# Kernel tuning notes

Hardware: AMD Instinct MI355X
Metric: run time of the kernel (lower is better)

The kernel has to match this reference:

```python
import jax, jax.numpy as jnp
import numpy as np

DT = 0.01  # init kwarg dt
M = 501    # microstructure feature length (hardcoded split [501, 501] in source)
H = 128    # hidden width


def _mlp(x, W1, b1, W2, b2):
    # Linear -> Softplus -> Linear
    return jax.nn.softplus(x @ W1 + b1) @ W2 + b2


def _linear_init(key, fan_in, fan_out):
    k1, k2 = jax.random.split(key)
    s = 1.0 / np.sqrt(fan_in)
    W = jax.random.uniform(k1, (fan_in, fan_out), minval=-s, maxval=s, dtype=jnp.float32)
    b = jax.random.uniform(k2, (fan_out,), minval=-s, maxval=s, dtype=jnp.float32)
    return W, b


def setup_inputs() -> dict:
    key = jax.random.key(0)
    ks = jax.random.split(key, 10)
    B, T = 32768, 512
    Ew1, Eb1 = _linear_init(ks[0], 2 * M, H)   # energy net: Linear(1002,128)
    Ew2, Eb2 = _linear_init(ks[1], H, 1)
    nw1, nb1 = _linear_init(ks[2], M, H)       # nu net: Linear(501,128)
    nw2, nb2 = _linear_init(ks[3], H, 1)
    bw1, bb1 = _linear_init(ks[4], 2 * M, H)   # beta net: Linear(1002,128)
    bw2, bb2 = _linear_init(ks[5], H, 1)
    e = jax.random.normal(ks[6], (B, T, 1), dtype=jnp.float32) * 0.01
    e_dot = jax.random.normal(ks[7], (B, T, 1), dtype=jnp.float32) * 0.01
    E = jax.random.uniform(ks[8], (B, M), dtype=jnp.float32)
    nu = jax.random.uniform(ks[9], (B, M), dtype=jnp.float32)
    return dict(e=e, e_dot=e_dot, E=E, nu=nu,
                Ew1=Ew1, Eb1=Eb1, Ew2=Ew2, Eb2=Eb2,
                nw1=nw1, nb1=nb1, nw2=nw2, nb2=nb2,
                bw1=bw1, bb1=bb1, bw2=bw2, bb2=bb2)


def reference(e, e_dot, E, nu,
              Ew1, Eb1, Ew2, Eb2,
              nw1, nb1, nw2, nb2,
              bw1, bb1, bw2, bb2):
    # microstructure encoder: m = concat(E, nu) -> [B, 1002]; constant over time,
    # so the three small MLPs are evaluated ONCE (the per-step autograd.grad of the
    # quadratic energy/dissipation potentials has closed form).
    m = jnp.concatenate((E, nu), axis=-1)
    Emod = jnp.exp(_mlp(m, Ew1, Eb1, Ew2, Eb2))                              # exp(E(m))    [B,1]
    nu_feat = m[:, M:]                                                        # second half of split
    nuv = jnp.exp(jnp.square(_mlp(nu_feat, nw1, nb1, nw2, nb2)) / 40000.0)    # exp(nu(.))   [B,1]
    beta = jnp.square(_mlp(m, bw1, bb1, bw2, bb2)) / 40000.0                  # beta(m)      [B,1]

    # Per-step closed-form derivatives of
    #   energy    = 1/2 exp(E(m)) u^2 + 1/2 (u - v)^2        (u = e_t, v = xi_t)
    #   potential = -1/2 exp(nu) p^2 + 1/2 sum(beta q^2)     (p = e_dot_t, q = -dE/dv = e_t - xi_t)
    #   s_eq = exp(E) u + (u - v);  s_neq = dPhi/dp = -exp(nu) p;  kinetics = dPhi/dq = beta q
    def step(xi, inputs):
        et, edt = inputs                     # [B,1] each
        q = et - xi
        stress_t = Emod * et + q + nuv * edt  # s_eq - s_neq
        xi_next = xi + DT * beta * q
        return xi_next, (stress_t, xi)

    xi0 = jnp.zeros_like(e[:, 0])            # [B,1]
    eT = jnp.moveaxis(e, 1, 0)               # [T,B,1]
    edT = jnp.moveaxis(e_dot, 1, 0)
    _, (stress, xi) = jax.lax.scan(step, xi0, (eT, edT))
    return jnp.moveaxis(stress, 0, 1), jnp.moveaxis(xi, 0, 1)  # [B,T,1] each
```

## Files before the change

### kernel.cpp

```cpp
#include <hip/hip_runtime.h>
#include <hip/hip_bf16.h>

#define M_ 501
#define T_ 512
#define DT_ 0.01f

typedef __attribute__((ext_vector_type(8))) __bf16 bf16x8;
typedef __attribute__((ext_vector_type(4))) float f32x4;

static __device__ __forceinline__ unsigned int pack2(float a, float b) {
    __hip_bfloat16 ha = __float2bfloat16(a);
    __hip_bfloat16 hb = __float2bfloat16(b);
    unsigned short ua = __builtin_bit_cast(unsigned short, ha);
    unsigned short ub = __builtin_bit_cast(unsigned short, hb);
    return (unsigned int)ua | ((unsigned int)ub << 16);
}

__global__ void build_w(const float* __restrict__ Ew1, const float* __restrict__ bw1,
                        const float* __restrict__ nw1, __hip_bfloat16* __restrict__ Wswz) {
    int idx = blockIdx.x * 256 + threadIdx.x;
    if (idx >= 32 * 24 * 64 * 8) return;
    int e  = idx & 7;
    int l  = (idx >> 3) & 63;
    int t  = idx >> 9;
    int nt = t % 24, k0 = t / 24;
    int k  = k0 * 32 + ((l >> 4) << 3) + e;
    int n  = nt * 16 + (l & 15);
    float v = 0.f;
    if (n < 128)      { if (k < 2*M_)             v = Ew1[k * 128 + n]; }
    else if (n < 256) { if (k < 2*M_)             v = bw1[k * 128 + (n - 128)]; }
    else              { if (k >= M_ && k < 2*M_)  v = nw1[(k - M_) * 128 + (n - 256)]; }
    Wswz[idx] = __float2bfloat16(v);
}

__global__ __launch_bounds__(512, 4) void fused_all(
    const float* __restrict__ E, const float* __restrict__ nu,
    const __hip_bfloat16* __restrict__ Wswz,
    const float* __restrict__ Eb1, const float* __restrict__ bb1, const float* __restrict__ nb1,
    const float* __restrict__ Ew2, const float* __restrict__ bw2, const float* __restrict__ nw2,
    const float* __restrict__ Eb2, const float* __restrict__ bb2, const float* __restrict__ nb2,
    const float* __restrict__ e, const float* __restrict__ ed,
    float* __restrict__ stress, float* __restrict__ xiout, int B)
{
    const int tid = threadIdx.x;
    const int wid = tid >> 6, l = tid & 63;
    const int c = l & 15, g = l >> 4;
    const int brow = blockIdx.x * 64;

    __shared__ __align__(16) unsigned char sAraw[2][64 * 128];
    __shared__ float cb1[384], cw2[384];
    __shared__ float lds_s[3][64];

    if (tid < 384) {
        int n = tid;
        cb1[n] = (n < 128) ? Eb1[n] : (n < 256) ? bb1[n - 128] : nb1[n - 256];
        cw2[n] = (n < 128) ? Ew2[n] : (n < 256) ? bw2[n - 128] : nw2[n - 256];
    }
    if (tid < 192) ((float*)lds_s)[tid] = 0.f;

    f32x4 q0, q1, q2; int ofs;
    const int sr = tid >> 3, su = tid & 7;
    const size_t rb = (size_t)(brow + sr) * M_;
    auto stage_load = [&](int ch) {
        int cu = ch * 8 + su;
        bool slow = (cu == 62) | (cu >= 124);
        if (!slow) {
            const float* src = (cu < 62) ? E : nu;
            int off = (cu < 62) ? cu * 8 : cu * 8 - M_;
            size_t s = rb + (size_t)off;
            ofs = (int)(s & 3);
            const f32x4* p = (const f32x4*)(src + (s & ~(size_t)3));
            q0 = p[0]; q1 = p[1]; q2 = p[2];
        } else {
            int kb = cu * 8;
            auto ldx = [&](int k) -> float {
                return (k < M_) ? E[rb + k] : ((k < 2 * M_) ? nu[rb + k - M_] : 0.f);
            };
            q0 = (f32x4){ldx(kb+0), ldx(kb+1), ldx(kb+2), ldx(kb+3)};
            q1 = (f32x4){ldx(kb+4), ldx(kb+5), ldx(kb+6), ldx(kb+7)};
            q2 = (f32x4){0.f, 0.f, 0.f, 0.f};
            ofs = 0;
        }
    };
    auto stage_finish = [&](int nbuf) {
        asm volatile("" : "+v"(q0), "+v"(q1), "+v"(q2));
        float g0=q0[0], g1=q0[1], g2=q0[2], g3=q0[3],
              g4=q1[0], g5=q1[1], g6=q1[2], g7=q1[3],
              g8=q2[0], g9=q2[1], g10=q2[2];
        const bool o2 = (ofs & 2) != 0, o1 = (ofs & 1) != 0;
        float u0 = o2?g2:g0, u1 = o2?g3:g1, u2 = o2?g4:g2, u3 = o2?g5:g3,
              u4 = o2?g6:g4, u5 = o2?g7:g5, u6 = o2?g8:g6, u7 = o2?g9:g7,
              u8 = o2?g10:g8;
        float f0 = o1?u1:u0, f1 = o1?u2:u1, f2 = o1?u3:u2, f3 = o1?u4:u3,
              f4 = o1?u5:u4, f5 = o1?u6:u5, f6 = o1?u7:u6, f7 = o1?u8:u7;
        uint4 vv;
        vv.x = pack2(f0, f1); vv.y = pack2(f2, f3);
        vv.z = pack2(f4, f5); vv.w = pack2(f6, f7);
        unsigned bo = ((unsigned)sr << 7) + ((((unsigned)su) << 4) ^ (((unsigned)(sr & 7)) << 4));
        *(uint4*)(sAraw[nbuf] + bo) = vv;
    };

    const bf16x8* wbase = (const bf16x8*)Wswz;
    auto loadW3 = [&](bf16x8 (&w)[3], int kg) {
        #pragma unroll
        for (int nt = 0; nt < 3; ++nt)
            w[nt] = wbase[(size_t)(kg * 24 + wid * 3 + nt) * 64 + l];
    };

    f32x4 acc[4][3];
    #pragma unroll
    for (int mi = 0; mi < 4; mi++)
        #pragma unroll
        for (int nt = 0; nt < 3; nt++) acc[mi][nt] = (f32x4){0.f, 0.f, 0.f, 0.f};
    bf16x8 wcur[3], wnxt[3], af[4];

    auto readAF = [&](int buf, int kk) {
        #pragma unroll
        for (int mi = 0; mi < 4; ++mi) {
            int row = c + mi * 16;
            unsigned bo = ((unsigned)row << 7) +
                ((((unsigned)kk << 6) + ((unsigned)g << 4)) ^ (((unsigned)(row & 7)) << 4));
            af[mi] = *(const bf16x8*)(sAraw[buf] + bo);
        }
    };
    auto M12 = [&](bf16x8 (&w)[3]) {
        #pragma unroll
        for (int nt = 0; nt < 3; ++nt)
            #pragma unroll
            for (int mi = 0; mi < 4; ++mi)
                acc[mi][nt] = __builtin_amdgcn_mfma_f32_16x16x32_bf16(w[nt], af[mi], acc[mi][nt], 0, 0, 0);
    };

    stage_load(0);
    loadW3(wcur, 0);
    stage_finish(0);
    __syncthreads();

    for (int ch = 0; ch < 16; ++ch) {
        const int buf = ch & 1;
        const int kg = ch * 2;
        loadW3(wnxt, kg + 1);
        if (ch < 15) stage_load(ch + 1);
        readAF(buf, 0); M12(wcur);
        if (ch < 15) loadW3(wcur, kg + 2);
        readAF(buf, 1); M12(wnxt);
        if (ch < 15) stage_finish(buf ^ 1);
        __syncthreads();
    }

    float bv[12], wv[12];
    #pragma unroll
    for (int nt = 0; nt < 3; ++nt)
        #pragma unroll
        for (int r = 0; r < 4; ++r) {
            int nidx = (wid * 3 + nt) * 16 + g * 4 + r;
            bv[nt * 4 + r] = cb1[nidx];
            wv[nt * 4 + r] = cw2[nidx];
        }
    const int m_first = (wid * 3) >> 3, m_last = (wid * 3 + 2) >> 3;

    #pragma unroll
    for (int mi = 0; mi < 4; ++mi) {
        float s0 = 0.f, s1 = 0.f, s2 = 0.f;
        #pragma unroll
        for (int nt = 0; nt < 3; ++nt) {
            float p = 0.f;
            #pragma unroll
            for (int r = 0; r < 4; ++r) {
                float x = acc[mi][nt][r] + bv[nt * 4 + r];
                float h = fmaxf(x, 0.f) + __logf(1.f + __expf(-fabsf(x)));
                p += h * wv[nt * 4 + r];
            }
            int m = (wid * 3 + nt) >> 3;
            if (m == 0) s0 += p; else if (m == 1) s1 += p; else s2 += p;
        }
        auto red = [&](float v, int m) {
            v += __shfl_xor(v, 16);
            v += __shfl_xor(v, 32);
            if (l < 16) atomicAdd(&lds_s[m][mi * 16 + l], v);
        };
        if (m_first == 0) red(s0, 0);
        if (m_first <= 1 && m_last >= 1) red(s1, 1);
        if (m_last == 2) red(s2, 2);
    }
    __syncthreads();

    if (tid < 64) {
        float s0 = lds_s[0][tid], s1 = lds_s[1][tid], s2 = lds_s[2][tid];
        lds_s[0][tid] = __expf(s0 + Eb2[0]);
        float mb = s1 + bb2[0];
        lds_s[1][tid] = mb * mb * (1.f / 40000.f);
        float mn = s2 + nb2[0];
        lds_s[2][tid] = __expf(mn * mn * (1.f / 40000.f));
    }
    __syncthreads();

    for (int i = 0; i < 8; ++i) {
        const int rr = wid * 8 + i;
        const int b = brow + rr;
        float Em = lds_s[0][rr], bt = lds_s[1][rr], nv = lds_s[2][rr];
        float cc = DT_ * bt;
        float a  = 1.f - cc;

        size_t base = (size_t)b * T_ + (size_t)l * 8;
        float4 e0 = *(const float4*)(e + base),  e1 = *(const float4*)(e + base + 4);
        float4 d0 = *(const float4*)(ed + base), d1 = *(const float4*)(ed + base + 4);
        float ev[8] = {e0.x, e0.y, e0.z, e0.w, e1.x, e1.y, e1.z, e1.w};
        float dv[8] = {d0.x, d0.y, d0.z, d0.w, d1.x, d1.y, d1.z, d1.w};

        float S = 0.f;
        #pragma unroll
        for (int j = 0; j < 8; j++) S = a * S + ev[j];
        float a2 = a * a, a4 = a2 * a2, A = a4 * a4;

        #pragma unroll
        for (int d = 1; d < 64; d <<= 1) {
            float Su = __shfl_up(S, d);
            float Au = __shfl_up(A, d);
            if (l >= d) { S = Su * A + S; A = Au * A; }
        }
        float Sp = __shfl_up(S, 1);
        float xi = (l == 0) ? 0.f : cc * Sp;

        float st[8], xo[8];
        #pragma unroll
        for (int j = 0; j < 8; j++) {
            xo[j] = xi;
            float qd = ev[j] - xi;
            st[j] = Em * ev[j] + qd + nv * dv[j];
            xi = xi + cc * qd;
        }
        *(float4*)(stress + base)     = (float4){st[0], st[1], st[2], st[3]};
        *(float4*)(stress + base + 4) = (float4){st[4], st[5], st[6], st[7]};
        *(float4*)(xiout + base)      = (float4){xo[0], xo[1], xo[2], xo[3]};
        *(float4*)(xiout + base + 4)  = (float4){xo[4], xo[5], xo[6], xo[7]};
    }
}

extern "C" void kernel_launch(void* const* d_in, const int* in_sizes, int n_in,
                              void* d_out, int out_size, void* d_ws, size_t ws_size,
                              hipStream_t stream) {
    const float* e   = (const float*)d_in[0];
    const float* ed  = (const float*)d_in[1];
    const float* E   = (const float*)d_in[2];
    const float* nu  = (const float*)d_in[3];
    const float* Ew1 = (const float*)d_in[4];
    const float* Eb1 = (const float*)d_in[5];
    const float* Ew2 = (const float*)d_in[6];
    const float* Eb2 = (const float*)d_in[7];
    const float* nw1 = (const float*)d_in[8];
    const float* nb1 = (const float*)d_in[9];
    const float* nw2 = (const float*)d_in[10];
    const float* nb2 = (const float*)d_in[11];
    const float* bw1 = (const float*)d_in[12];
    const float* bb1 = (const float*)d_in[13];
    const float* bw2 = (const float*)d_in[14];
    const float* bb2 = (const float*)d_in[15];

    int B = in_sizes[2] / M_;

    char* ws = (char*)d_ws;
    __hip_bfloat16* Wswz = (__hip_bfloat16*)ws;

    float* stress = (float*)d_out;
    float* xiout  = stress + (size_t)B * T_;

    build_w<<<(1024 * 384 + 255) / 256, 256, 0, stream>>>(Ew1, bw1, nw1, Wswz);
    fused_all<<<B / 64, 512, 0, stream>>>(E, nu, Wswz, Eb1, bb1, nb1,
                                          Ew2, bw2, nw2, Eb2, bb2, nb2,
                                          e, ed, stress, xiout, B);
}
```

Before: 110.9 us.

## Stage bf16 microstructure tile through global scratch instead of LDS double buffer

Replaces the LDS double-buffered pipeline, which converted E/nu to bf16 and interleaved it with the MFMA loop, with a prologue. The prologue converts the block's whole 64-row input tile to bf16 and writes it to a global workspace buffer, then a fence and barrier follow. The MFMA loop then reads A fragments straight from that global (L2-resident) buffer with no per-chunk barriers. It also drops the launch-bounds occupancy hint from 4 to 2. This removes LDS use and per-iteration syncs, but adds a global write/read round trip, loses the overlap of loads with compute, and may cost occupancy.

```diff
diff --git a/kernel.cpp b/kernel.cpp
--- a/kernel.cpp
+++ b/kernel.cpp
@@ -33,9 +33,9 @@
     Wswz[idx] = __float2bfloat16(v);
 }
 
-__global__ __launch_bounds__(512, 4) void fused_all(
+__global__ __launch_bounds__(512, 2) void fused_all(
     const float* __restrict__ E, const float* __restrict__ nu,
-    const __hip_bfloat16* __restrict__ Wswz,
+    const __hip_bfloat16* __restrict__ Wswz, __hip_bfloat16* __restrict__ Xt,
     const float* __restrict__ Eb1, const float* __restrict__ bb1, const float* __restrict__ nb1,
     const float* __restrict__ Ew2, const float* __restrict__ bw2, const float* __restrict__ nw2,
     const float* __restrict__ Eb2, const float* __restrict__ bb2, const float* __restrict__ nb2,
@@ -47,7 +47,6 @@
     const int c = l & 15, g = l >> 4;
     const int brow = blockIdx.x * 64;
 
-    __shared__ __align__(16) unsigned char sAraw[2][64 * 128];
     __shared__ float cb1[384], cw2[384];
     __shared__ float lds_s[3][64];
 
@@ -58,94 +57,68 @@
     }
     if (tid < 192) ((float*)lds_s)[tid] = 0.f;
 
-    f32x4 q0, q1, q2; int ofs;
-    const int sr = tid >> 3, su = tid & 7;
-    const size_t rb = (size_t)(brow + sr) * M_;
-    auto stage_load = [&](int ch) {
-        int cu = ch * 8 + su;
-        bool slow = (cu == 62) | (cu >= 124);
-        if (!slow) {
-            const float* src = (cu < 62) ? E : nu;
-            int off = (cu < 62) ? cu * 8 : cu * 8 - M_;
-            size_t s = rb + (size_t)off;
-            ofs = (int)(s & 3);
-            const f32x4* p = (const f32x4*)(src + (s & ~(size_t)3));
-            q0 = p[0]; q1 = p[1]; q2 = p[2];
-        } else {
-            int kb = cu * 8;
-            auto ldx = [&](int k) -> float {
-                return (k < M_) ? E[rb + k] : ((k < 2 * M_) ? nu[rb + k - M_] : 0.f);
-            };
-            q0 = (f32x4){ldx(kb+0), ldx(kb+1), ldx(kb+2), ldx(kb+3)};
-            q1 = (f32x4){ldx(kb+4), ldx(kb+5), ldx(kb+6), ldx(kb+7)};
-            q2 = (f32x4){0.f, 0.f, 0.f, 0.f};
-            ofs = 0;
-        }
-    };
-    auto stage_finish = [&](int nbuf) {
-        asm volatile("" : "+v"(q0), "+v"(q1), "+v"(q2));
-        float g0=q0[0], g1=q0[1], g2=q0[2], g3=q0[3],
-              g4=q1[0], g5=q1[1], g6=q1[2], g7=q1[3],
-              g8=q2[0], g9=q2[1], g10=q2[2];
-        const bool o2 = (ofs & 2) != 0, o1 = (ofs & 1) != 0;
-        float u0 = o2?g2:g0, u1 = o2?g3:g1, u2 = o2?g4:g2, u3 = o2?g5:g3,
-              u4 = o2?g6:g4, u5 = o2?g7:g5, u6 = o2?g8:g6, u7 = o2?g9:g7,
-              u8 = o2?g10:g8;
-        float f0 = o1?u1:u0, f1 = o1?u2:u1, f2 = o1?u3:u2, f3 = o1?u4:u3,
-              f4 = o1?u5:u4, f5 = o1?u6:u5, f6 = o1?u7:u6, f7 = o1?u8:u7;
-        uint4 vv;
-        vv.x = pack2(f0, f1); vv.y = pack2(f2, f3);
-        vv.z = pack2(f4, f5); vv.w = pack2(f6, f7);
-        unsigned bo = ((unsigned)sr << 7) + ((((unsigned)su) << 4) ^ (((unsigned)(sr & 7)) << 4));
-        *(uint4*)(sAraw[nbuf] + bo) = vv;
-    };
+    {
+        const int sr = tid >> 3, su = tid & 7;
+        const size_t rb = (size_t)(brow + sr) * M_;
+        for (int ch = 0; ch < 16; ++ch) {
+            const int cu = ch * 8 + su;
+            float f0, f1, f2, f3, f4, f5, f6, f7;
+            const bool slow = (cu == 62) | (cu >= 124);
+            if (!slow) {
+                const float* src = (cu < 62) ? E : nu;
+                const int off = (cu < 62) ? cu * 8 : cu * 8 - M_;
+                const size_t s = rb + (size_t)off;
+                const int o = (int)(s & 3);
+                const f32x4* p = (const f32x4*)(src + (s & ~(size_t)3));
+                f32x4 q0 = p[0], q1 = p[1], q2 = p[2];
+                asm volatile("" : "+v"(q0), "+v"(q1), "+v"(q2));
+                float g0=q0[0], g1=q0[1], g2=q0[2], g3=q0[3],
+                      g4=q1[0], g5=q1[1], g6=q1[2], g7=q1[3],
+                      g8=q2[0], g9=q2[1], g10=q2[2];
+                const bool o2 = (o & 2) != 0, o1 = (o & 1) != 0;
+                float u0 = o2?g2:g0, u1 = o2?g3:g1, u2 = o2?g4:g2, u3 = o2?g5:g3,
+                      u4 = o2?g6:g4, u5 = o2?g7:g5, u6 = o2?g8:g6, u7 = o2?g9:g7,
+                      u8 = o2?g10:g8;
+                f0 = o1?u1:u0; f1 = o1?u2:u1; f2 = o1?u3:u2; f3 = o1?u4:u3;
+                f4 = o1?u5:u4; f5 = o1?u6:u5; f6 = o1?u7:u6; f7 = o1?u8:u7;
+            } else {
+                const int kb = cu * 8;
+                auto ldx = [&](int k) -> float {
+                    return (k < M_) ? E[rb + k] : ((k < 2 * M_) ? nu[rb + k - M_] : 0.f);
+                };
+                f0 = ldx(kb+0); f1 = ldx(kb+1); f2 = ldx(kb+2); f3 = ldx(kb+3);
+                f4 = ldx(kb+4); f5 = ldx(kb+5); f6 = ldx(kb+6); f7 = ldx(kb+7);
+            }
+            uint4 vv;
+            vv.x = pack2(f0, f1); vv.y = pack2(f2, f3);
+            vv.z = pack2(f4, f5); vv.w = pack2(f6, f7);
+            *(uint4*)(Xt + ((size_t)(cu >> 2) * B + brow + sr) * 32 + (cu & 3) * 8) = vv;
+        }
+    }
+    __threadfence();
+    __syncthreads();
 
     const bf16x8* wbase = (const bf16x8*)Wswz;
-    auto loadW3 = [&](bf16x8 (&w)[3], int kg) {
-        #pragma unroll
-        for (int nt = 0; nt < 3; ++nt)
-            w[nt] = wbase[(size_t)(kg * 24 + wid * 3 + nt) * 64 + l];
-    };
-
     f32x4 acc[4][3];
     #pragma unroll
     for (int mi = 0; mi < 4; mi++)
         #pragma unroll
         for (int nt = 0; nt < 3; nt++) acc[mi][nt] = (f32x4){0.f, 0.f, 0.f, 0.f};
-    bf16x8 wcur[3], wnxt[3], af[4];
-
-    auto readAF = [&](int buf, int kk) {
-        #pragma unroll
-        for (int mi = 0; mi < 4; ++mi) {
-            int row = c + mi * 16;
-            unsigned bo = ((unsigned)row << 7) +
-                ((((unsigned)kk << 6) + ((unsigned)g << 4)) ^ (((unsigned)(row & 7)) << 4));
-            af[mi] = *(const bf16x8*)(sAraw[buf] + bo);
-        }
-    };
-    auto M12 = [&](bf16x8 (&w)[3]) {
+
+    for (int kg = 0; kg < 32; ++kg) {
+        bf16x8 w[3];
+        #pragma unroll
+        for (int nt = 0; nt < 3; ++nt)
+            w[nt] = wbase[(size_t)(kg * 24 + wid * 3 + nt) * 64 + l];
+        bf16x8 af[4];
+        #pragma unroll
+        for (int mi = 0; mi < 4; ++mi)
+            af[mi] = *(const bf16x8*)(Xt + ((size_t)kg * B + brow + c + mi * 16) * 32 + g * 8);
         #pragma unroll
         for (int nt = 0; nt < 3; ++nt)
             #pragma unroll
             for (int mi = 0; mi < 4; ++mi)
                 acc[mi][nt] = __builtin_amdgcn_mfma_f32_16x16x32_bf16(w[nt], af[mi], acc[mi][nt], 0, 0, 0);
-    };
-
-    stage_load(0);
-    loadW3(wcur, 0);
-    stage_finish(0);
-    __syncthreads();
-
-    for (int ch = 0; ch < 16; ++ch) {
-        const int buf = ch & 1;
-        const int kg = ch * 2;
-        loadW3(wnxt, kg + 1);
-        if (ch < 15) stage_load(ch + 1);
-        readAF(buf, 0); M12(wcur);
-        if (ch < 15) loadW3(wcur, kg + 2);
-        readAF(buf, 1); M12(wnxt);
-        if (ch < 15) stage_finish(buf ^ 1);
-        __syncthreads();
     }
 
     float bv[12], wv[12];
@@ -261,12 +234,13 @@
 
     char* ws = (char*)d_ws;
     __hip_bfloat16* Wswz = (__hip_bfloat16*)ws;
+    __hip_bfloat16* Xt   = (__hip_bfloat16*)(ws + 786432);
 
     float* stress = (float*)d_out;
     float* xiout  = stress + (size_t)B * T_;
 
     build_w<<<(1024 * 384 + 255) / 256, 256, 0, stream>>>(Ew1, bw1, nw1, Wswz);
-    fused_all<<<B / 64, 512, 0, stream>>>(E, nu, Wswz, Eb1, bb1, nb1,
+    fused_all<<<B / 64, 512, 0, stream>>>(E, nu, Wswz, Xt, Eb1, bb1, nb1,
                                           Ew2, bw2, nw2, Eb2, bb2, nb2,
                                           e, ed, stress, xiout, B);
 }
```

Measured after the change: 247.1 us. +122.8%, slower.

## Triple-buffer LDS A tiles with two-deep global prefetch in fused MLP GEMM

Applied to the files above, without the earlier changes.

Replaces the double-buffered LDS staging of the microstructure activations with a three-buffer ring and two sets of in-flight prefetch registers, so global loads run two chunks ahead of compute. The weight register prefetch is removed and weights are loaded inline per k-group. Barriers become a raw s_barrier plus sched_barrier after an lgkmcnt wait. Launch bounds drop from 4 to 2 waves-per-EU occupancy, giving more registers per thread at the cost of fewer resident blocks.

```diff
diff --git a/kernel.cpp b/kernel.cpp
--- a/kernel.cpp
+++ b/kernel.cpp
@@ -33,7 +33,7 @@
     Wswz[idx] = __float2bfloat16(v);
 }
 
-__global__ __launch_bounds__(512, 4) void fused_all(
+__global__ __launch_bounds__(512, 2) void fused_all(
     const float* __restrict__ E, const float* __restrict__ nu,
     const __hip_bfloat16* __restrict__ Wswz,
     const float* __restrict__ Eb1, const float* __restrict__ bb1, const float* __restrict__ nb1,
@@ -47,7 +47,7 @@
     const int c = l & 15, g = l >> 4;
     const int brow = blockIdx.x * 64;
 
-    __shared__ __align__(16) unsigned char sAraw[2][64 * 128];
+    __shared__ __align__(16) unsigned char sAraw[3][64 * 128];
     __shared__ float cb1[384], cw2[384];
     __shared__ float lds_s[3][64];
 
@@ -58,36 +58,37 @@
     }
     if (tid < 192) ((float*)lds_s)[tid] = 0.f;
 
-    f32x4 q0, q1, q2; int ofs;
     const int sr = tid >> 3, su = tid & 7;
     const size_t rb = (size_t)(brow + sr) * M_;
-    auto stage_load = [&](int ch) {
+    f32x4 qa0, qa1, qa2, qb0, qb1, qb2; int oa = 0, ob = 0;
+
+    auto stage_load = [&](int ch, f32x4& r0, f32x4& r1, f32x4& r2, int& ro) {
         int cu = ch * 8 + su;
         bool slow = (cu == 62) | (cu >= 124);
         if (!slow) {
             const float* src = (cu < 62) ? E : nu;
             int off = (cu < 62) ? cu * 8 : cu * 8 - M_;
             size_t s = rb + (size_t)off;
-            ofs = (int)(s & 3);
+            ro = (int)(s & 3);
             const f32x4* p = (const f32x4*)(src + (s & ~(size_t)3));
-            q0 = p[0]; q1 = p[1]; q2 = p[2];
+            r0 = p[0]; r1 = p[1]; r2 = p[2];
         } else {
             int kb = cu * 8;
             auto ldx = [&](int k) -> float {
                 return (k < M_) ? E[rb + k] : ((k < 2 * M_) ? nu[rb + k - M_] : 0.f);
             };
-            q0 = (f32x4){ldx(kb+0), ldx(kb+1), ldx(kb+2), ldx(kb+3)};
-            q1 = (f32x4){ldx(kb+4), ldx(kb+5), ldx(kb+6), ldx(kb+7)};
-            q2 = (f32x4){0.f, 0.f, 0.f, 0.f};
-            ofs = 0;
+            r0 = (f32x4){ldx(kb+0), ldx(kb+1), ldx(kb+2), ldx(kb+3)};
+            r1 = (f32x4){ldx(kb+4), ldx(kb+5), ldx(kb+6), ldx(kb+7)};
+            r2 = (f32x4){0.f, 0.f, 0.f, 0.f};
+            ro = 0;
         }
     };
-    auto stage_finish = [&](int nbuf) {
-        asm volatile("" : "+v"(q0), "+v"(q1), "+v"(q2));
-        float g0=q0[0], g1=q0[1], g2=q0[2], g3=q0[3],
-              g4=q1[0], g5=q1[1], g6=q1[2], g7=q1[3],
-              g8=q2[0], g9=q2[1], g10=q2[2];
-        const bool o2 = (ofs & 2) != 0, o1 = (ofs & 1) != 0;
+    auto stage_finish = [&](int nbuf, f32x4& r0, f32x4& r1, f32x4& r2, int& ro) {
+        asm volatile("" : "+v"(r0), "+v"(r1), "+v"(r2));
+        float g0=r0[0], g1=r0[1], g2=r0[2], g3=r0[3],
+              g4=r1[0], g5=r1[1], g6=r1[2], g7=r1[3],
+              g8=r2[0], g9=r2[1], g10=r2[2];
+        const bool o2 = (ro & 2) != 0, o1 = (ro & 1) != 0;
         float u0 = o2?g2:g0, u1 = o2?g3:g1, u2 = o2?g4:g2, u3 = o2?g5:g3,
               u4 = o2?g6:g4, u5 = o2?g7:g5, u6 = o2?g8:g6, u7 = o2?g9:g7,
               u8 = o2?g10:g8;
@@ -101,52 +102,62 @@
     };
 
     const bf16x8* wbase = (const bf16x8*)Wswz;
-    auto loadW3 = [&](bf16x8 (&w)[3], int kg) {
-        #pragma unroll
-        for (int nt = 0; nt < 3; ++nt)
-            w[nt] = wbase[(size_t)(kg * 24 + wid * 3 + nt) * 64 + l];
-    };
 
     f32x4 acc[4][3];
     #pragma unroll
     for (int mi = 0; mi < 4; mi++)
         #pragma unroll
         for (int nt = 0; nt < 3; nt++) acc[mi][nt] = (f32x4){0.f, 0.f, 0.f, 0.f};
-    bf16x8 wcur[3], wnxt[3], af[4];
-
-    auto readAF = [&](int buf, int kk) {
-        #pragma unroll
-        for (int mi = 0; mi < 4; ++mi) {
-            int row = c + mi * 16;
-            unsigned bo = ((unsigned)row << 7) +
-                ((((unsigned)kk << 6) + ((unsigned)g << 4)) ^ (((unsigned)(row & 7)) << 4));
-            af[mi] = *(const bf16x8*)(sAraw[buf] + bo);
+
+    auto compute = [&](int bufi, int ch) {
+        #pragma unroll
+        for (int kk = 0; kk < 2; ++kk) {
+            const int kg = ch * 2 + kk;
+            bf16x8 w[3];
+            #pragma unroll
+            for (int nt = 0; nt < 3; ++nt)
+                w[nt] = wbase[(size_t)(kg * 24 + wid * 3 + nt) * 64 + l];
+            bf16x8 af[4];
+            #pragma unroll
+            for (int mi = 0; mi < 4; ++mi) {
+                int row = c + mi * 16;
+                unsigned bo = ((unsigned)row << 7) +
+                    ((((unsigned)kk << 6) + ((unsigned)g << 4)) ^ (((unsigned)(row & 7)) << 4));
+                af[mi] = *(const bf16x8*)(sAraw[bufi] + bo);
+            }
+            #pragma unroll
+            for (int nt = 0; nt < 3; ++nt)
+                #pragma unroll
+                for (int mi = 0; mi < 4; ++mi)
+                    acc[mi][nt] = __builtin_amdgcn_mfma_f32_16x16x32_bf16(w[nt], af[mi], acc[mi][nt], 0, 0, 0);
         }
     };
-    auto M12 = [&](bf16x8 (&w)[3]) {
-        #pragma unroll
-        for (int nt = 0; nt < 3; ++nt)
-            #pragma unroll
-            for (int mi = 0; mi < 4; ++mi)
-                acc[mi][nt] = __builtin_amdgcn_mfma_f32_16x16x32_bf16(w[nt], af[mi], acc[mi][nt], 0, 0, 0);
-    };
-
-    stage_load(0);
-    loadW3(wcur, 0);
-    stage_finish(0);
-    __syncthreads();
-
-    for (int ch = 0; ch < 16; ++ch) {
-        const int buf = ch & 1;
-        const int kg = ch * 2;
-        loadW3(wnxt, kg + 1);
-        if (ch < 15) stage_load(ch + 1);
-        readAF(buf, 0); M12(wcur);
-        if (ch < 15) loadW3(wcur, kg + 2);
-        readAF(buf, 1); M12(wnxt);
-        if (ch < 15) stage_finish(buf ^ 1);
-        __syncthreads();
-    }
+
+    #define BAR() do {                                        \
+        asm volatile("s_waitcnt lgkmcnt(0)" ::: "memory");    \
+        __builtin_amdgcn_s_barrier();                         \
+        __builtin_amdgcn_sched_barrier(0);                    \
+    } while (0)
+
+    stage_load(0, qa0, qa1, qa2, oa);
+    stage_load(1, qb0, qb1, qb2, ob);
+    stage_finish(0, qa0, qa1, qa2, oa);
+    stage_load(2, qa0, qa1, qa2, oa);
+    stage_finish(1, qb0, qb1, qb2, ob);
+    BAR();
+
+    for (int ch = 0; ch < 16; ch += 2) {
+        compute(ch % 3, ch);
+        if (ch + 3 < 16) stage_load(ch + 3, qb0, qb1, qb2, ob);
+        if (ch + 2 < 16) stage_finish((ch + 2) % 3, qa0, qa1, qa2, oa);
+        BAR();
+        const int c1 = ch + 1;
+        compute(c1 % 3, c1);
+        if (c1 + 3 < 16) stage_load(c1 + 3, qa0, qa1, qa2, oa);
+        if (c1 + 2 < 16) stage_finish((c1 + 2) % 3, qb0, qb1, qb2, ob);
+        BAR();
+    }
+    #undef BAR
 
     float bv[12], wv[12];
     #pragma unroll
```

New measurement: 136.2 us. 1.23x slower.

## Swizzle block order, raise MFMA priority, and pair rows in scan epilogue

Applied to the files above, without the earlier changes.

Remaps block IDs so consecutive blocks go to different XCDs (bid&7 stride), which spreads row ranges across chiplets. Wraps the MFMA burst in s_setprio to favour matrix issue over other waves. Processes two batch rows at once in the time-scan epilogue, doubling independent loads, shuffles and stores in flight to hide memory latency. The swizzle assumes the grid is exactly 512 blocks (B=32768/64); any other grid size would index the wrong rows, and the paired epilogue raises register pressure.

```diff
diff --git a/kernel.cpp b/kernel.cpp
--- a/kernel.cpp
+++ b/kernel.cpp
@@ -45,7 +45,9 @@
     const int tid = threadIdx.x;
     const int wid = tid >> 6, l = tid & 63;
     const int c = l & 15, g = l >> 4;
-    const int brow = blockIdx.x * 64;
+    const int bid = blockIdx.x;
+    const int swz = (bid & 7) * 64 + (bid >> 3);
+    const int brow = swz * 64;
 
     __shared__ __align__(16) unsigned char sAraw[2][64 * 128];
     __shared__ float cb1[384], cw2[384];
@@ -124,11 +126,13 @@
         }
     };
     auto M12 = [&](bf16x8 (&w)[3]) {
+        __builtin_amdgcn_s_setprio(1);
         #pragma unroll
         for (int nt = 0; nt < 3; ++nt)
             #pragma unroll
             for (int mi = 0; mi < 4; ++mi)
                 acc[mi][nt] = __builtin_amdgcn_mfma_f32_16x16x32_bf16(w[nt], af[mi], acc[mi][nt], 0, 0, 0);
+        __builtin_amdgcn_s_setprio(0);
     };
 
     stage_load(0);
@@ -195,45 +199,60 @@
     }
     __syncthreads();
 
-    for (int i = 0; i < 8; ++i) {
-        const int rr = wid * 8 + i;
-        const int b = brow + rr;
-        float Em = lds_s[0][rr], bt = lds_s[1][rr], nv = lds_s[2][rr];
-        float cc = DT_ * bt;
-        float a  = 1.f - cc;
-
-        size_t base = (size_t)b * T_ + (size_t)l * 8;
-        float4 e0 = *(const float4*)(e + base),  e1 = *(const float4*)(e + base + 4);
-        float4 d0 = *(const float4*)(ed + base), d1 = *(const float4*)(ed + base + 4);
-        float ev[8] = {e0.x, e0.y, e0.z, e0.w, e1.x, e1.y, e1.z, e1.w};
-        float dv[8] = {d0.x, d0.y, d0.z, d0.w, d1.x, d1.y, d1.z, d1.w};
-
-        float S = 0.f;
-        #pragma unroll
-        for (int j = 0; j < 8; j++) S = a * S + ev[j];
-        float a2 = a * a, a4 = a2 * a2, A = a4 * a4;
+    #pragma unroll
+    for (int pi = 0; pi < 4; ++pi) {
+        const int rA = wid * 8 + pi * 2, rB = rA + 1;
+        const int bA = brow + rA, bB = brow + rB;
+        float EmA = lds_s[0][rA], btA = lds_s[1][rA], nvA = lds_s[2][rA];
+        float EmB = lds_s[0][rB], btB = lds_s[1][rB], nvB = lds_s[2][rB];
+        float ccA = DT_ * btA, aA = 1.f - ccA;
+        float ccB = DT_ * btB, aB = 1.f - ccB;
+
+        size_t baA = (size_t)bA * T_ + (size_t)l * 8;
+        size_t baB = (size_t)bB * T_ + (size_t)l * 8;
+        float4 eA0 = *(const float4*)(e + baA),  eA1 = *(const float4*)(e + baA + 4);
+        float4 eB0 = *(const float4*)(e + baB),  eB1 = *(const float4*)(e + baB + 4);
+        float4 dA0 = *(const float4*)(ed + baA), dA1 = *(const float4*)(ed + baA + 4);
+        float4 dB0 = *(const float4*)(ed + baB), dB1 = *(const float4*)(ed + baB + 4);
+        float evA[8] = {eA0.x,eA0.y,eA0.z,eA0.w, eA1.x,eA1.y,eA1.z,eA1.w};
+        float evB[8] = {eB0.x,eB0.y,eB0.z,eB0.w, eB1.x,eB1.y,eB1.z,eB1.w};
+        float dvA[8] = {dA0.x,dA0.y,dA0.z,dA0.w, dA1.x,dA1.y,dA1.z,dA1.w};
+        float dvB[8] = {dB0.x,dB0.y,dB0.z,dB0.w, dB1.x,dB1.y,dB1.z,dB1.w};
+
+        float SA = 0.f, SB = 0.f;
+        #pragma unroll
+        for (int j = 0; j < 8; j++) { SA = aA * SA + evA[j]; SB = aB * SB + evB[j]; }
+        float a2A = aA*aA, AA = (a2A*a2A)*(a2A*a2A);
+        float a2B = aB*aB, AB = (a2B*a2B)*(a2B*a2B);
 
         #pragma unroll
         for (int d = 1; d < 64; d <<= 1) {
-            float Su = __shfl_up(S, d);
-            float Au = __shfl_up(A, d);
-            if (l >= d) { S = Su * A + S; A = Au * A; }
-        }
-        float Sp = __shfl_up(S, 1);
-        float xi = (l == 0) ? 0.f : cc * Sp;
-
-        float st[8], xo[8];
+            float SuA = __shfl_up(SA, d), AuA = __shfl_up(AA, d);
+            float SuB = __shfl_up(SB, d), AuB = __shfl_up(AB, d);
+            if (l >= d) { SA = SuA * AA + SA; AA = AuA * AA;
+                          SB = SuB * AB + SB; AB = AuB * AB; }
+        }
+        float SpA = __shfl_up(SA, 1), SpB = __shfl_up(SB, 1);
+        float xiA = (l == 0) ? 0.f : ccA * SpA;
+        float xiB = (l == 0) ? 0.f : ccB * SpB;
+
+        float stA[8], xoA[8], stB[8], xoB[8];
         #pragma unroll
         for (int j = 0; j < 8; j++) {
-            xo[j] = xi;
-            float qd = ev[j] - xi;
-            st[j] = Em * ev[j] + qd + nv * dv[j];
-            xi = xi + cc * qd;
-        }
-        *(float4*)(stress + base)     = (float4){st[0], st[1], st[2], st[3]};
-        *(float4*)(stress + base + 4) = (float4){st[4], st[5], st[6], st[7]};
-        *(float4*)(xiout + base)      = (float4){xo[0], xo[1], xo[2], xo[3]};
-        *(float4*)(xiout + base + 4)  = (float4){xo[4], xo[5], xo[6], xo[7]};
+            xoA[j] = xiA; xoB[j] = xiB;
+            float qA = evA[j] - xiA, qB = evB[j] - xiB;
+            stA[j] = EmA * evA[j] + qA + nvA * dvA[j];
+            stB[j] = EmB * evB[j] + qB + nvB * dvB[j];
+            xiA += ccA * qA; xiB += ccB * qB;
+        }
+        *(float4*)(stress + baA)     = (float4){stA[0],stA[1],stA[2],stA[3]};
+        *(float4*)(stress + baA + 4) = (float4){stA[4],stA[5],stA[6],stA[7]};
+        *(float4*)(stress + baB)     = (float4){stB[0],stB[1],stB[2],stB[3]};
+        *(float4*)(stress + baB + 4) = (float4){stB[4],stB[5],stB[6],stB[7]};
+        *(float4*)(xiout + baA)      = (float4){xoA[0],xoA[1],xoA[2],xoA[3]};
+        *(float4*)(xiout + baA + 4)  = (float4){xoA[4],xoA[5],xoA[6],xoA[7]};
+        *(float4*)(xiout + baB)      = (float4){xoB[0],xoB[1],xoB[2],xoB[3]};
+        *(float4*)(xiout + baB + 4)  = (float4){xoB[4],xoB[5],xoB[6],xoB[7]};
     }
 }
 
```

New measurement: 111.1 us. Within noise of the previous version (+0.2%).
